# Optimization experiments

Measured on AMD Instinct MI355X. Metric: run time of the kernel, lower is better.

The kernel has to match this reference:

```python
import jax, jax.numpy as jnp
import numpy as np

D_MODEL = 2048
N_HEAD = 16
HEAD_DIM = D_MODEL // N_HEAD
FFN_DIM = 4 * D_MODEL
B, T = 2, 2048
EPS = float(np.finfo(np.float32).eps)  # torch nn.RMSNorm default eps


def _rmsnorm(x, w):
    return x * jax.lax.rsqrt(jnp.mean(x * x, axis=-1, keepdims=True) + EPS) * w


def _apply_rope(x, cos, sin):
    # x: (B,H,T,hd); cos/sin: (T,hd) with each frequency repeated twice
    cos_pair = cos[..., 0::2]
    sin_pair = sin[..., 0::2]
    x_even = x[..., 0::2]
    x_odd = x[..., 1::2]
    rot_even = x_even * cos_pair - x_odd * sin_pair
    rot_odd = x_odd * cos_pair + x_even * sin_pair
    # interleave back: (..., hd//2, 2) -> (..., hd)
    return jnp.stack([rot_even, rot_odd], axis=-1).reshape(x.shape)


def setup_inputs() -> dict:
    key = jax.random.key(0)
    ks = jax.random.split(key, 9)
    x = jax.random.normal(ks[0], (B, T, D_MODEL), dtype=jnp.float32)
    # real RoPE cache: freqs repeated twice along last axis (interleaved-pair)
    inv_freq = 1.0 / (10000.0 ** (np.arange(0, HEAD_DIM, 2, dtype=np.float32) / HEAD_DIM))
    ang = np.arange(T, dtype=np.float32)[:, None] * inv_freq[None, :]  # (T, hd/2)
    ang2 = np.repeat(ang, 2, axis=-1)  # (T, hd)
    rope_cache = jnp.stack([jnp.cos(jnp.asarray(ang2)), jnp.sin(jnp.asarray(ang2))], axis=0)
    s = 0.02
    return {
        "x": x,
        "rope_cache": rope_cache,
        "attn_norm_w": jnp.ones((D_MODEL,), jnp.float32),
        "qkv_w": s * jax.random.normal(ks[1], (3 * D_MODEL, D_MODEL), jnp.float32),
        "q_norm_w": jnp.ones((HEAD_DIM,), jnp.float32),
        "k_norm_w": jnp.ones((HEAD_DIM,), jnp.float32),
        "out_proj_w": s * jax.random.normal(ks[2], (D_MODEL, D_MODEL), jnp.float32),
        "mlp_norm_w": jnp.ones((D_MODEL,), jnp.float32),
        "mlp_in_w": s * jax.random.normal(ks[3], (FFN_DIM, D_MODEL), jnp.float32),
        "mlp_out_w": s * jax.random.normal(ks[4], (D_MODEL, FFN_DIM), jnp.float32),
    }


def reference(x, rope_cache, attn_norm_w, qkv_w, q_norm_w, k_norm_w,
              out_proj_w, mlp_norm_w, mlp_in_w, mlp_out_w):
    cos, sin = rope_cache[0], rope_cache[1]
    b, t, d = x.shape
    h = _rmsnorm(x, attn_norm_w)
    qkv = h @ qkv_w.T  # (B,T,3D)
    q, k, v = jnp.split(qkv, 3, axis=-1)
    q = q.reshape(b, t, N_HEAD, HEAD_DIM).transpose(0, 2, 1, 3)
    k = k.reshape(b, t, N_HEAD, HEAD_DIM).transpose(0, 2, 1, 3)
    v = v.reshape(b, t, N_HEAD, HEAD_DIM).transpose(0, 2, 1, 3)
    q = _rmsnorm(_apply_rope(q, cos, sin), q_norm_w)
    k = _rmsnorm(_apply_rope(k, cos, sin), k_norm_w)
    scale = 1.0 / jnp.sqrt(jnp.float32(HEAD_DIM))
    scores = jnp.einsum('bhqd,bhkd->bhqk', q, k) * scale
    causal = jnp.tril(jnp.ones((t, t), dtype=bool))
    scores = jnp.where(causal, scores, -jnp.inf)
    attn = jax.nn.softmax(scores, axis=-1)
    attn_out = jnp.einsum('bhqk,bhkd->bhqd', attn, v)
    attn_out = attn_out.transpose(0, 2, 1, 3).reshape(b, t, d)
    x = x + attn_out @ out_proj_w.T
    m = _rmsnorm(x, mlp_norm_w) @ mlp_in_w.T
    m = jnp.square(jax.nn.relu(m))
    return x + m @ mlp_out_w.T
```

## Files before the change

### kernel.cpp

```cpp
#include <hip/hip_runtime.h>
#include <stdint.h>

#define TT 2048
#define DM 2048
#define NH 16
#define HD 128
#define FFN 8192
#define MR 4096
#define EPSF 1.1920928955078125e-07f
#define NEGBIG (-1.0e30f)

typedef __attribute__((ext_vector_type(8))) short short8;
typedef __attribute__((ext_vector_type(4))) float f32x4;
typedef unsigned short u16;
typedef unsigned int u32;

__device__ __forceinline__ float bf2f(u32 u) {
    return __uint_as_float((u & 0xffffu) << 16);
}
__device__ __forceinline__ u16 f2bf(float f) {
    u32 x = __float_as_uint(f);
    return (u16)((x + 0x7fffu + ((x >> 16) & 1u)) >> 16);
}
__device__ __forceinline__ void load8f(const u16* p, float* v) {
    uint4 d = *(const uint4*)p;
    v[0] = bf2f(d.x); v[1] = bf2f(d.x >> 16);
    v[2] = bf2f(d.y); v[3] = bf2f(d.y >> 16);
    v[4] = bf2f(d.z); v[5] = bf2f(d.z >> 16);
    v[6] = bf2f(d.w); v[7] = bf2f(d.w >> 16);
}
__device__ __forceinline__ void load8f32(const float* p, float* v) {
    float4 a = *(const float4*)p, b = *(const float4*)(p + 4);
    v[0]=a.x; v[1]=a.y; v[2]=a.z; v[3]=a.w; v[4]=b.x; v[5]=b.y; v[6]=b.z; v[7]=b.w;
}
__device__ __forceinline__ void store8bf(u16* p, const float* v) {
    uint4 o;
    o.x = (u32)f2bf(v[0]) | ((u32)f2bf(v[1]) << 16);
    o.y = (u32)f2bf(v[2]) | ((u32)f2bf(v[3]) << 16);
    o.z = (u32)f2bf(v[4]) | ((u32)f2bf(v[5]) << 16);
    o.w = (u32)f2bf(v[6]) | ((u32)f2bf(v[7]) << 16);
    *(uint4*)p = o;
}
__device__ __forceinline__ uint4 cvt8_f32_bf16(const float* p) {
    float4 a = *(const float4*)p, b = *(const float4*)(p + 4);
    uint4 o;
    o.x = (u32)f2bf(a.x) | ((u32)f2bf(a.y) << 16);
    o.y = (u32)f2bf(a.z) | ((u32)f2bf(a.w) << 16);
    o.z = (u32)f2bf(b.x) | ((u32)f2bf(b.y) << 16);
    o.w = (u32)f2bf(b.z) | ((u32)f2bf(b.w) << 16);
    return o;
}
__device__ __forceinline__ void gload_lds16(const void* g, void* l) {
    __builtin_amdgcn_global_load_lds((const __attribute__((address_space(1))) u32*)g,
                                     (__attribute__((address_space(3))) u32*)l, 16, 0, 0);
}

__global__ __launch_bounds__(256)
void cvt_w(const float* __restrict__ S, u16* __restrict__ D) {
    size_t i = ((size_t)blockIdx.x * 256 + threadIdx.x) * 8;
    *(uint4*)(D + i) = cvt8_f32_bf16(S + i);
}

__global__ __launch_bounds__(256)
void rmsnorm_k(const float* __restrict__ X, const float* __restrict__ W, u16* __restrict__ O) {
    const int row = blockIdx.x, tid = threadIdx.x;
    float v[8];
    load8f32(X + (size_t)row * DM + tid * 8, v);
    float ssq = 0.f;
#pragma unroll
    for (int i = 0; i < 8; ++i) ssq += v[i] * v[i];
#pragma unroll
    for (int d = 1; d < 64; d <<= 1) ssq += __shfl_xor(ssq, d);
    __shared__ float red[4];
    if ((tid & 63) == 0) red[tid >> 6] = ssq;
    __syncthreads();
    ssq = red[0] + red[1] + red[2] + red[3];
    const float inv = rsqrtf(ssq * (1.f / DM) + EPSF);
    float wv[8], o[8];
    load8f32(W + tid * 8, wv);
#pragma unroll
    for (int i = 0; i < 8; ++i) o[i] = v[i] * inv * wv[i];
    store8bf(O + (size_t)row * DM + tid * 8, o);
}

template<int EPI>
__global__ __launch_bounds__(256, 2)
void gemm_ring(const u16* __restrict__ A, const u16* __restrict__ Bw,
               const float* __restrict__ Res, void* __restrict__ Cp,
               int M, int N, int K, int ldb) {
    __shared__ alignas(16) u16 As[4][128 * 32];
    __shared__ alignas(16) u16 Bs[4][128 * 32];
    const int tid = threadIdx.x;
    const int lane = tid & 63, w = tid >> 6;
    const int quad = lane >> 4, col = lane & 15;
    const int n0 = blockIdx.x * 128, m0 = blockIdx.y * 128;
    const int wm = (w >> 1) * 64, wn = (w & 1) * 64;

    const int c0 = tid, c1 = tid + 256;
    const int ar0 = c0 >> 2, aq0 = (c0 & 3) ^ ((ar0 >> 1) & 3);
    const int ar1 = c1 >> 2, aq1 = (c1 & 3) ^ ((ar1 >> 1) & 3);
    const u16* agp0 = A  + (size_t)(m0 + ar0) * K + aq0 * 8;
    const u16* agp1 = A  + (size_t)(m0 + ar1) * K + aq1 * 8;
    const u16* bgp0 = Bw + (size_t)(n0 + ar0) * ldb + aq0 * 8;
    const u16* bgp1 = Bw + (size_t)(n0 + ar1) * ldb + aq1 * 8;
    const int l0 = c0 * 8, l1 = c1 * 8;

    int aoff[4], boff[4];
#pragma unroll
    for (int i = 0; i < 4; ++i) {
        int r = wm + i * 16 + col;
        aoff[i] = r * 32 + (quad ^ ((r >> 1) & 3)) * 8;
        r = wn + i * 16 + col;
        boff[i] = r * 32 + (quad ^ ((r >> 1) & 3)) * 8;
    }

    f32x4 acc[4][4];
#pragma unroll
    for (int i = 0; i < 4; ++i)
#pragma unroll
        for (int j = 0; j < 4; ++j) acc[i][j] = (f32x4){0.f, 0.f, 0.f, 0.f};

    const int KT = K >> 5;

#define GR_STAGE(s) { const int _b = (s) & 3; const size_t _ko = (size_t)(s) * 32; \
    gload_lds16(agp0 + _ko, &As[_b][l0]); \
    gload_lds16(agp1 + _ko, &As[_b][l1]); \
    gload_lds16(bgp0 + _ko, &Bs[_b][l0]); \
    gload_lds16(bgp1 + _ko, &Bs[_b][l1]); }

    GR_STAGE(0);
    GR_STAGE(1);
    GR_STAGE(2);

    asm volatile("s_waitcnt vmcnt(8)" ::: "memory");
    __builtin_amdgcn_s_barrier();
    short8 af[4], bfr[4];
#pragma unroll
    for (int i = 0; i < 4; ++i) af[i]  = *(const short8*)(As[0] + aoff[i]);
#pragma unroll
    for (int i = 0; i < 4; ++i) bfr[i] = *(const short8*)(Bs[0] + boff[i]);

    for (int t = 0; t < KT; ++t) {
        if (t <= KT - 3) asm volatile("s_waitcnt vmcnt(4)" ::: "memory");
        else             asm volatile("s_waitcnt vmcnt(0)" ::: "memory");
        __builtin_amdgcn_s_barrier();
        if (t + 3 < KT) GR_STAGE(t + 3);
        const u16* abn = As[(t + 1) & 3];
        const u16* bbn = Bs[(t + 1) & 3];
        short8 bfr2[4];
        __builtin_amdgcn_s_setprio(1);
#pragma unroll
        for (int mi = 0; mi < 4; ++mi) {
#pragma unroll
            for (int ni = 0; ni < 4; ++ni)
                acc[mi][ni] = __builtin_amdgcn_mfma_f32_16x16x32_bf16(af[mi], bfr[ni], acc[mi][ni], 0, 0, 0);
            bfr2[mi] = *(const short8*)(bbn + boff[mi]);
            af[mi]   = *(const short8*)(abn + aoff[mi]);
        }
        __builtin_amdgcn_s_setprio(0);
#pragma unroll
        for (int ni = 0; ni < 4; ++ni) bfr[ni] = bfr2[ni];
        __builtin_amdgcn_sched_barrier(0);
    }
#undef GR_STAGE

#pragma unroll
    for (int mi = 0; mi < 4; ++mi)
#pragma unroll
        for (int ni = 0; ni < 4; ++ni) {
            const int rbase = m0 + wm + mi * 16 + quad * 4;
            const int cc = n0 + wn + ni * 16 + col;
#pragma unroll
            for (int rr = 0; rr < 4; ++rr) {
                float v = acc[mi][ni][rr];
                size_t idx = (size_t)(rbase + rr) * N + cc;
                if (EPI == 0) ((u16*)Cp)[idx] = f2bf(v);
                else if (EPI == 1) { float t2 = fmaxf(v, 0.f); ((u16*)Cp)[idx] = f2bf(t2 * t2); }
                else ((float*)Cp)[idx] = v + Res[idx];
            }
        }
}

template<int EPI>
__global__ __launch_bounds__(512, 2)
void gemm_big(const u16* __restrict__ A, const u16* __restrict__ Bw,
              void* __restrict__ Cp, int M, int N, int K, int ldb) {
    __shared__ alignas(16) u16 As[4][256 * 32];
    __shared__ alignas(16) u16 Bs[4][256 * 32];
    const int tid = threadIdx.x;
    const int lane = tid & 63, w = tid >> 6;
    const int wr = w >> 2, wc = w & 3;
    const int quad = lane >> 4, colL = lane & 15;

    const int nbx = N >> 8;
    const int nwg = gridDim.x;
    const int cpx = nwg >> 3;
    const int bid = blockIdx.x;
    const int swz = (bid & 7) * cpx + (bid >> 3);
    const int by = swz / nbx, bx = swz - by * nbx;
    const int m0 = by << 8, n0 = bx << 8;

    const int r0 = tid >> 2,       q0 = (tid & 3) ^ ((r0 >> 1) & 3);
    const int p1 = tid + 512;
    const int r1 = p1 >> 2,        q1 = (p1 & 3) ^ ((r1 >> 1) & 3);
    const u16* agp0 = A  + (size_t)(m0 + r0) * K   + q0 * 8;
    const u16* agp1 = A  + (size_t)(m0 + r1) * K   + q1 * 8;
    const u16* bgp0 = Bw + (size_t)(n0 + r0) * ldb + q0 * 8;
    const u16* bgp1 = Bw + (size_t)(n0 + r1) * ldb + q1 * 8;
    const int l0 = tid * 8, l1 = p1 * 8;

    int aoff[8], boff[4];
#pragma unroll
    for (int mi = 0; mi < 8; ++mi) {
        int r = wr * 128 + mi * 16 + colL;
        aoff[mi] = r * 32 + (quad ^ ((r >> 1) & 3)) * 8;
    }
#pragma unroll
    for (int ni = 0; ni < 4; ++ni) {
        int r = wc * 64 + ni * 16 + colL;
        boff[ni] = r * 32 + (quad ^ ((r >> 1) & 3)) * 8;
    }

    f32x4 acc[8][4];
#pragma unroll
    for (int i = 0; i < 8; ++i)
#pragma unroll
        for (int j = 0; j < 4; ++j) acc[i][j] = (f32x4){0.f, 0.f, 0.f, 0.f};

    const int KT = K >> 5;

#define GB_STAGE(s) { const int _b = (s) & 3; const size_t _ko = (size_t)(s) * 32; \
    gload_lds16(agp0 + _ko, &As[_b][l0]); \
    gload_lds16(agp1 + _ko, &As[_b][l1]); \
    gload_lds16(bgp0 + _ko, &Bs[_b][l0]); \
    gload_lds16(bgp1 + _ko, &Bs[_b][l1]); }

    GB_STAGE(0);
    GB_STAGE(1);
    GB_STAGE(2);

    asm volatile("s_waitcnt vmcnt(8)" ::: "memory");
    __builtin_amdgcn_s_barrier();
    short8 af[8], bfr[4];
#pragma unroll
    for (int i = 0; i < 8; ++i) af[i]  = *(const short8*)(As[0] + aoff[i]);
#pragma unroll
    for (int i = 0; i < 4; ++i) bfr[i] = *(const short8*)(Bs[0] + boff[i]);

    for (int t = 0; t < KT; ++t) {
        if (t <= KT - 3) asm volatile("s_waitcnt vmcnt(4)" ::: "memory");
        else             asm volatile("s_waitcnt vmcnt(0)" ::: "memory");
        __builtin_amdgcn_s_barrier();
        if (t + 3 < KT) GB_STAGE(t + 3);
        const u16* abn = As[(t + 1) & 3];
        const u16* bbn = Bs[(t + 1) & 3];
        short8 bfr2[4];
        __builtin_amdgcn_s_setprio(1);
#pragma unroll
        for (int mi = 0; mi < 8; ++mi) {
#pragma unroll
            for (int ni = 0; ni < 4; ++ni)
                acc[mi][ni] = __builtin_amdgcn_mfma_f32_16x16x32_bf16(af[mi], bfr[ni], acc[mi][ni], 0, 0, 0);
            if (mi < 4) bfr2[mi] = *(const short8*)(bbn + boff[mi]);
            af[mi] = *(const short8*)(abn + aoff[mi]);
        }
        __builtin_amdgcn_s_setprio(0);
#pragma unroll
        for (int ni = 0; ni < 4; ++ni) bfr[ni] = bfr2[ni];
        __builtin_amdgcn_sched_barrier(0);
    }
#undef GB_STAGE

#pragma unroll
    for (int mi = 0; mi < 8; ++mi)
#pragma unroll
        for (int ni = 0; ni < 4; ++ni) {
            const int rbase = m0 + wr * 128 + mi * 16 + quad * 4;
            const int cc = n0 + wc * 64 + ni * 16 + colL;
#pragma unroll
            for (int rr = 0; rr < 4; ++rr) {
                float v = acc[mi][ni][rr];
                size_t idx = (size_t)(rbase + rr) * N + cc;
                if (EPI == 0) ((u16*)Cp)[idx] = f2bf(v);
                else { float tq = fmaxf(v, 0.f); ((u16*)Cp)[idx] = f2bf(tq * tq); }
            }
        }
}

__global__ __launch_bounds__(256)
void rope_split_k(const u16* __restrict__ QKV, const float* __restrict__ RC,
                  const float* __restrict__ QW, const float* __restrict__ KW,
                  u16* __restrict__ Qo, u16* __restrict__ Ko, u16* __restrict__ Vo) {
    const int row = blockIdx.x;
    const int t = row & (TT - 1), b = row >> 11;
    const int tid = threadIdx.x, h = tid >> 4, j = tid & 15;
    const size_t qb = (size_t)row * (3 * DM) + h * HD + j * 8;
    float q[8], k[8], cs[8], sn[8];
    load8f(QKV + qb, q);
    load8f(QKV + qb + DM, k);
    uint4 vv = *(const uint4*)(QKV + qb + 2 * DM);
    load8f32(RC + (size_t)t * HD + j * 8, cs);
    load8f32(RC + (size_t)(TT + t) * HD + j * 8, sn);
    float qr[8], kr[8];
#pragma unroll
    for (int p = 0; p < 4; ++p) {
        float c = cs[2 * p], s = sn[2 * p];
        qr[2*p]   = q[2*p]   * c - q[2*p+1] * s;
        qr[2*p+1] = q[2*p+1] * c + q[2*p]   * s;
        kr[2*p]   = k[2*p]   * c - k[2*p+1] * s;
        kr[2*p+1] = k[2*p+1] * c + k[2*p]   * s;
    }
    float sq = 0.f, sk = 0.f;
#pragma unroll
    for (int i = 0; i < 8; ++i) { sq += qr[i] * qr[i]; sk += kr[i] * kr[i]; }
#pragma unroll
    for (int d = 1; d < 16; d <<= 1) { sq += __shfl_xor(sq, d); sk += __shfl_xor(sk, d); }
    const float iq = rsqrtf(sq * (1.f / HD) + EPSF);
    const float ik = rsqrtf(sk * (1.f / HD) + EPSF);
    float qw[8], kw[8], oq[8], ok[8];
    load8f32(QW + j * 8, qw); load8f32(KW + j * 8, kw);
#pragma unroll
    for (int i = 0; i < 8; ++i) { oq[i] = qr[i] * iq * qw[i]; ok[i] = kr[i] * ik * kw[i]; }
    const size_t ob = ((size_t)(b * NH + h) * TT + t) * HD + j * 8;
    store8bf(Qo + ob, oq);
    store8bf(Ko + ob, ok);
    *(uint4*)(Vo + ob) = vv;
}

__global__ __launch_bounds__(256)
void transpose_v(const u16* __restrict__ V, u16* __restrict__ Vt) {
    __shared__ alignas(16) u16 tile[64][72];
    const int bh = blockIdx.z;
    const int t0 = blockIdx.x * 64, d0 = blockIdx.y * 64;
    const int tid = threadIdx.x;
#pragma unroll
    for (int i = 0; i < 2; ++i) {
        int c = i * 256 + tid;
        int r = c >> 3, cc = (c & 7) * 8;
        *(uint4*)(&tile[r][cc]) = *(const uint4*)(V + ((size_t)bh * TT + t0 + r) * HD + d0 + cc);
    }
    __syncthreads();
#pragma unroll
    for (int i = 0; i < 2; ++i) {
        int c = i * 256 + tid;
        int dc = c >> 3, rr = (c & 7) * 8;
        u16 tmp[8];
#pragma unroll
        for (int kk = 0; kk < 8; ++kk) tmp[kk] = tile[rr + kk][dc];
        uint4 o;
        o.x = (u32)tmp[0] | ((u32)tmp[1] << 16);
        o.y = (u32)tmp[2] | ((u32)tmp[3] << 16);
        o.z = (u32)tmp[4] | ((u32)tmp[5] << 16);
        o.w = (u32)tmp[6] | ((u32)tmp[7] << 16);
        *(uint4*)(Vt + ((size_t)bh * HD + d0 + dc) * TT + t0 + rr) = o;
    }
}

__global__ __launch_bounds__(256, 2)
void attn_k(const u16* __restrict__ Q, const u16* __restrict__ Kg,
            const u16* __restrict__ Vt, u16* __restrict__ O) {
    __shared__ alignas(16) u16 k_lds[2][64 * 128];
    __shared__ alignas(16) u16 v_lds[2][128 * 64];
    __shared__ alignas(16) u16 p_lds[128 * 40];
    const int bh = blockIdx.x;
    const int yy = blockIdx.y;
    const int qt = (yy < 8) ? (15 - yy) : (yy - 8);
    const int tid = threadIdx.x, lane = tid & 63, w = tid >> 6;
    const int quad = lane >> 4, col = lane & 15;
    const int qbase = qt * 128;
    const int wq = qbase + w * 32;

    short8 qf[2][4];
#pragma unroll
    for (int sub = 0; sub < 2; ++sub) {
        const u16* qp = Q + ((size_t)bh * TT + wq + sub * 16 + col) * HD;
#pragma unroll
        for (int s = 0; s < 4; ++s) qf[sub][s] = *(const short8*)(qp + s * 32 + quad * 8);
    }
    short8 ones8;
#pragma unroll
    for (int j = 0; j < 8; ++j) ones8[j] = (short)0x3F80;

    const u16* kp[4]; const u16* vp[4];
#pragma unroll
    for (int i = 0; i < 4; ++i) {
        int lin = i * 256 + tid;
        int r = lin >> 4, sl = lin & 15;
        int gq = sl ^ (r & 15);
        kp[i] = Kg + ((size_t)bh * TT + r) * HD + gq * 8;
    }
#pragma unroll
    for (int i = 0; i < 4; ++i) {
        int lin = i * 256 + tid;
        int r = lin >> 3, sl = lin & 7;
        int gq = sl ^ (r & 7);
        vp[i] = Vt + ((size_t)bh * HD + r) * TT + gq * 8;
    }

    f32x4 oacc[2][8];
#pragma unroll
    for (int s = 0; s < 2; ++s)
#pragma unroll
        for (int i = 0; i < 8; ++i) oacc[s][i] = (f32x4){0.f, 0.f, 0.f, 0.f};
    float mrow[2][4], lrow[2][4];
#pragma unroll
    for (int s = 0; s < 2; ++s)
#pragma unroll
        for (int r = 0; r < 4; ++r) { mrow[s][r] = NEGBIG; lrow[s][r] = 0.f; }
    const float scale = 0.08838834764831845f;

    u16* kcur = k_lds[0]; u16* knxt = k_lds[1];
    u16* vcur = v_lds[0]; u16* vnxt = v_lds[1];
#pragma unroll
    for (int i = 0; i < 4; ++i) gload_lds16(kp[i], kcur + (i * 256 + tid) * 8);
#pragma unroll
    for (int i = 0; i < 4; ++i) gload_lds16(vp[i], vcur + (i * 256 + tid) * 8);

    const int ktmax = 2 * qt + 1;
    for (int kt = 0; kt <= ktmax; ++kt) {
        const int kb = kt * 64;
        __syncthreads();

        if (kt < ktmax) {
            const int kb2 = kb + 64;
#pragma unroll
            for (int i = 0; i < 4; ++i) gload_lds16(kp[i] + (size_t)kb2 * HD, knxt + (i * 256 + tid) * 8);
#pragma unroll
            for (int i = 0; i < 4; ++i) gload_lds16(vp[i] + kb2, vnxt + (i * 256 + tid) * 8);
        }

        f32x4 sfr[2][4];
#pragma unroll
        for (int s = 0; s < 2; ++s)
#pragma unroll
            for (int ni = 0; ni < 4; ++ni) sfr[s][ni] = (f32x4){0.f, 0.f, 0.f, 0.f};
        __builtin_amdgcn_s_setprio(1);
#pragma unroll
        for (int ni = 0; ni < 4; ++ni) {
            const int r = ni * 16 + col;
#pragma unroll
            for (int s = 0; s < 4; ++s) {
                int sl = (s * 4 + quad) ^ (r & 15);
                short8 kf = *(const short8*)(kcur + r * 128 + sl * 8);
                sfr[0][ni] = __builtin_amdgcn_mfma_f32_16x16x32_bf16(qf[0][s], kf, sfr[0][ni], 0, 0, 0);
                sfr[1][ni] = __builtin_amdgcn_mfma_f32_16x16x32_bf16(qf[1][s], kf, sfr[1][ni], 0, 0, 0);
            }
        }
        __builtin_amdgcn_s_setprio(0);
#pragma unroll
        for (int sub = 0; sub < 2; ++sub)
#pragma unroll
            for (int ni = 0; ni < 4; ++ni) {
                const int key = kb + ni * 16 + col;
#pragma unroll
                for (int rr = 0; rr < 4; ++rr) {
                    float v = sfr[sub][ni][rr] * scale;
                    int qv = wq + sub * 16 + quad * 4 + rr;
                    if (key > qv) v = NEGBIG;
                    sfr[sub][ni][rr] = v;
                }
            }
        float mx[2][4];
#pragma unroll
        for (int sub = 0; sub < 2; ++sub)
#pragma unroll
            for (int rr = 0; rr < 4; ++rr)
                mx[sub][rr] = fmaxf(fmaxf(sfr[sub][0][rr], sfr[sub][1][rr]),
                                    fmaxf(sfr[sub][2][rr], sfr[sub][3][rr]));
#pragma unroll
        for (int d = 1; d < 16; d <<= 1)
#pragma unroll
            for (int sub = 0; sub < 2; ++sub)
#pragma unroll
                for (int rr = 0; rr < 4; ++rr) mx[sub][rr] = fmaxf(mx[sub][rr], __shfl_xor(mx[sub][rr], d));
        bool grew = false;
#pragma unroll
        for (int sub = 0; sub < 2; ++sub)
#pragma unroll
            for (int rr = 0; rr < 4; ++rr) grew = grew || (mx[sub][rr] > mrow[sub][rr]);
        if (__any(grew)) {
#pragma unroll
            for (int sub = 0; sub < 2; ++sub)
#pragma unroll
                for (int rr = 0; rr < 4; ++rr) {
                    float mn = fmaxf(mrow[sub][rr], mx[sub][rr]);
                    float a = __expf(mrow[sub][rr] - mn);
                    mrow[sub][rr] = mn;
                    lrow[sub][rr] *= a;
#pragma unroll
                    for (int i = 0; i < 8; ++i) oacc[sub][i][rr] *= a;
                }
        }
#pragma unroll
        for (int sub = 0; sub < 2; ++sub)
#pragma unroll
            for (int ni = 0; ni < 4; ++ni)
#pragma unroll
                for (int rr = 0; rr < 4; ++rr)
                    sfr[sub][ni][rr] = __expf(sfr[sub][ni][rr] - mrow[sub][rr]);
        f32x4 sacc[2];
        sacc[0] = (f32x4){0.f, 0.f, 0.f, 0.f};
        sacc[1] = (f32x4){0.f, 0.f, 0.f, 0.f};
#pragma unroll
        for (int ks = 0; ks < 2; ++ks) {
#pragma unroll
            for (int sub = 0; sub < 2; ++sub)
#pragma unroll
                for (int nio = 0; nio < 2; ++nio) {
                    const int ni = ks * 2 + nio;
#pragma unroll
                    for (int rr = 0; rr < 4; ++rr)
                        p_lds[(w * 32 + sub * 16 + quad * 4 + rr) * 40 + nio * 16 + col] = f2bf(sfr[sub][ni][rr]);
                }
            short8 pa0 = *(const short8*)(p_lds + (w * 32 + col) * 40 + quad * 8);
            short8 pa1 = *(const short8*)(p_lds + (w * 32 + 16 + col) * 40 + quad * 8);
            __builtin_amdgcn_s_setprio(1);
#pragma unroll
            for (int di = 0; di < 8; ++di) {
                int r = di * 16 + col;
                int sl = (ks * 4 + quad) ^ (r & 7);
                short8 vb = *(const short8*)(vcur + r * 64 + sl * 8);
                oacc[0][di] = __builtin_amdgcn_mfma_f32_16x16x32_bf16(pa0, vb, oacc[0][di], 0, 0, 0);
                oacc[1][di] = __builtin_amdgcn_mfma_f32_16x16x32_bf16(pa1, vb, oacc[1][di], 0, 0, 0);
            }
            sacc[0] = __builtin_amdgcn_mfma_f32_16x16x32_bf16(pa0, ones8, sacc[0], 0, 0, 0);
            sacc[1] = __builtin_amdgcn_mfma_f32_16x16x32_bf16(pa1, ones8, sacc[1], 0, 0, 0);
            __builtin_amdgcn_s_setprio(0);
        }
#pragma unroll
        for (int sub = 0; sub < 2; ++sub)
#pragma unroll
            for (int rr = 0; rr < 4; ++rr) lrow[sub][rr] += sacc[sub][rr];
        { u16* t = kcur; kcur = knxt; knxt = t; }
        { u16* t = vcur; vcur = vnxt; vnxt = t; }
    }
    const int b = bh >> 4, hh = bh & 15;
#pragma unroll
    for (int sub = 0; sub < 2; ++sub)
#pragma unroll
        for (int di = 0; di < 8; ++di)
#pragma unroll
            for (int rr = 0; rr < 4; ++rr) {
                int trow = wq + sub * 16 + quad * 4 + rr;
                float ov = oacc[sub][di][rr] / lrow[sub][rr];
                O[((size_t)(b * TT + trow)) * DM + hh * HD + di * 16 + col] = f2bf(ov);
            }
}

extern "C" void kernel_launch(void* const* d_in, const int* in_sizes, int n_in,
                              void* d_out, int out_size, void* d_ws, size_t ws_size,
                              hipStream_t stream) {
    const float* x    = (const float*)d_in[0];
    const float* rc   = (const float*)d_in[1];
    const float* anw  = (const float*)d_in[2];
    const float* qkvw = (const float*)d_in[3];
    const float* qnw  = (const float*)d_in[4];
    const float* knw  = (const float*)d_in[5];
    const float* opw  = (const float*)d_in[6];
    const float* mnw  = (const float*)d_in[7];
    const float* miw  = (const float*)d_in[8];
    const float* mow  = (const float*)d_in[9];

    char* ws = (char*)d_ws;
    u16* hbuf = (u16*)(ws);
    u16* Wq   = (u16*)(ws + (16ll  << 20));
    u16* Wmi  = (u16*)(ws + (16ll  << 20));
    u16* vt   = (u16*)(ws + (16ll  << 20));
    u16* aout = (u16*)(ws + (32ll  << 20));
    u16* Wmo  = (u16*)(ws + (48ll  << 20));
    u16* qkv  = (u16*)(ws + (48ll  << 20));
    u16* mbuf = (u16*)(ws + (80ll  << 20));
    u16* qh   = (u16*)(ws + (96ll  << 20));
    u16* Wo   = (u16*)(ws + (112ll << 20));
    u16* kh   = (u16*)(ws + (112ll << 20));
    u16* vh   = (u16*)(ws);
    float* xo = (float*)d_out;

    rmsnorm_k<<<MR, 256, 0, stream>>>(x, anw, hbuf);
    cvt_w<<<6144, 256, 0, stream>>>(qkvw, Wq);
    gemm_ring<0><<<dim3(48, 32), 256, 0, stream>>>(hbuf, Wq, nullptr, qkv, MR, 3 * DM, DM, DM);
    rope_split_k<<<MR, 256, 0, stream>>>(qkv, rc, qnw, knw, qh, kh, vh);
    transpose_v<<<dim3(32, 2, 32), 256, 0, stream>>>(vh, vt);
    attn_k<<<dim3(32, 16), 256, 0, stream>>>(qh, kh, vt, aout);
    cvt_w<<<2048, 256, 0, stream>>>(opw, Wo);
    cvt_w<<<8192, 256, 0, stream>>>(mow, Wmo);
    gemm_ring<2><<<dim3(16, 32), 256, 0, stream>>>(aout, Wo, x, xo, MR, DM, DM, DM);
    rmsnorm_k<<<MR, 256, 0, stream>>>(xo, mnw, hbuf);
    cvt_w<<<8192, 256, 0, stream>>>(miw, Wmi);
    gemm_big<1><<<256, 512, 0, stream>>>(hbuf, Wmi, mbuf, MR, FFN / 2, DM, DM);
    gemm_ring<2><<<dim3(16, 32), 256, 0, stream>>>(mbuf, Wmo, xo, xo, MR, DM, FFN / 2, FFN);
    gemm_big<1><<<256, 512, 0, stream>>>(hbuf, Wmi + (size_t)(FFN / 2) * DM, mbuf, MR, FFN / 2, DM, DM);
    gemm_ring<2><<<dim3(16, 32), 256, 0, stream>>>(mbuf, Wmo + FFN / 2, xo, xo, MR, DM, FFN / 2, FFN);
}
```

Measured before the change: 865.1 us.

## Shrink GEMM ring to three LDS stages and raise occupancy to three blocks

Cuts the GEMM shared-memory ring from four stages to three, dropping LDS per block from 64KB to 48KB, and raises launch bounds so three blocks can share a CU. It also removes the register double-buffering of A/B fragments, so fragments are now loaded from LDS at the top of each k-step instead of being prefetched during the MFMAs. The aim is more waves to hide latency, at the cost of a shallower prefetch depth and LDS reads that are no longer overlapped within a wave.

```diff
diff --git a/kernel.cpp b/kernel.cpp
--- a/kernel.cpp
+++ b/kernel.cpp
@@ -84,12 +84,12 @@
 }
 
 template<int EPI>
-__global__ __launch_bounds__(256, 2)
+__global__ __launch_bounds__(256, 3)
 void gemm_ring(const u16* __restrict__ A, const u16* __restrict__ Bw,
                const float* __restrict__ Res, void* __restrict__ Cp,
                int M, int N, int K, int ldb) {
-    __shared__ alignas(16) u16 As[4][128 * 32];
-    __shared__ alignas(16) u16 Bs[4][128 * 32];
+    __shared__ alignas(16) u16 As[3][128 * 32];
+    __shared__ alignas(16) u16 Bs[3][128 * 32];
     const int tid = threadIdx.x;
     const int lane = tid & 63, w = tid >> 6;
     const int quad = lane >> 4, col = lane & 15;
@@ -122,45 +122,38 @@
 
     const int KT = K >> 5;
 
-#define GR_STAGE(s) { const int _b = (s) & 3; const size_t _ko = (size_t)(s) * 32; \
-    gload_lds16(agp0 + _ko, &As[_b][l0]); \
-    gload_lds16(agp1 + _ko, &As[_b][l1]); \
-    gload_lds16(bgp0 + _ko, &Bs[_b][l0]); \
-    gload_lds16(bgp1 + _ko, &Bs[_b][l1]); }
-
-    GR_STAGE(0);
-    GR_STAGE(1);
-    GR_STAGE(2);
-
-    asm volatile("s_waitcnt vmcnt(8)" ::: "memory");
-    __builtin_amdgcn_s_barrier();
-    short8 af[4], bfr[4];
-#pragma unroll
-    for (int i = 0; i < 4; ++i) af[i]  = *(const short8*)(As[0] + aoff[i]);
-#pragma unroll
-    for (int i = 0; i < 4; ++i) bfr[i] = *(const short8*)(Bs[0] + boff[i]);
-
+#define GR_STAGE(s, b) { const size_t _ko = (size_t)(s) * 32; \
+    gload_lds16(agp0 + _ko, &As[b][l0]); \
+    gload_lds16(agp1 + _ko, &As[b][l1]); \
+    gload_lds16(bgp0 + _ko, &Bs[b][l0]); \
+    gload_lds16(bgp1 + _ko, &Bs[b][l1]); }
+
+    GR_STAGE(0, 0);
+    GR_STAGE(1, 1);
+
+    int bufc = 0, bufn = 2;
     for (int t = 0; t < KT; ++t) {
-        if (t <= KT - 3) asm volatile("s_waitcnt vmcnt(4)" ::: "memory");
-        else             asm volatile("s_waitcnt vmcnt(0)" ::: "memory");
+        if (t < KT - 1) asm volatile("s_waitcnt vmcnt(4)" ::: "memory");
+        else            asm volatile("s_waitcnt vmcnt(0)" ::: "memory");
         __builtin_amdgcn_s_barrier();
-        if (t + 3 < KT) GR_STAGE(t + 3);
-        const u16* abn = As[(t + 1) & 3];
-        const u16* bbn = Bs[(t + 1) & 3];
-        short8 bfr2[4];
+        if (t + 2 < KT) GR_STAGE(t + 2, bufn);
+        const u16* ab = As[bufc];
+        const u16* bb = Bs[bufc];
+        short8 af[4], bfr[4];
+#pragma unroll
+        for (int i = 0; i < 4; ++i) af[i]  = *(const short8*)(ab + aoff[i]);
+#pragma unroll
+        for (int i = 0; i < 4; ++i) bfr[i] = *(const short8*)(bb + boff[i]);
         __builtin_amdgcn_s_setprio(1);
 #pragma unroll
-        for (int mi = 0; mi < 4; ++mi) {
+        for (int mi = 0; mi < 4; ++mi)
 #pragma unroll
             for (int ni = 0; ni < 4; ++ni)
                 acc[mi][ni] = __builtin_amdgcn_mfma_f32_16x16x32_bf16(af[mi], bfr[ni], acc[mi][ni], 0, 0, 0);
-            bfr2[mi] = *(const short8*)(bbn + boff[mi]);
-            af[mi]   = *(const short8*)(abn + aoff[mi]);
-        }
         __builtin_amdgcn_s_setprio(0);
-#pragma unroll
-        for (int ni = 0; ni < 4; ++ni) bfr[ni] = bfr2[ni];
         __builtin_amdgcn_sched_barrier(0);
+        bufc = (bufc == 2) ? 0 : bufc + 1;
+        bufn = (bufn == 2) ? 0 : bufn + 1;
     }
 #undef GR_STAGE
 
```

Result: no change. 878.4 us (+1.5%).
